# Optimization experiments

Hardware: AMD Instinct MI355X
Metric: run time of the kernel (lower is better)

Reference implementation:

```python
import jax, jax.numpy as jnp
import numpy as np

D_MODEL = 512
NUM_HEADS = 8
HEAD_DIM = D_MODEL // NUM_HEADS
LN_EPS = 1e-5


def setup_inputs() -> dict:
    key = jax.random.key(0)
    ks = jax.random.split(key, 12)
    B, S, D = 4, 8192, D_MODEL
    scale = 1.0 / np.sqrt(D)  # xavier-ish init
    inp = {
        "x": jax.random.normal(ks[0], (B, S, D), dtype=jnp.float32),
        "Wq": jax.random.normal(ks[1], (D, D), dtype=jnp.float32) * scale,
        "bq": jnp.zeros((D,), dtype=jnp.float32),
        "Wk": jax.random.normal(ks[2], (D, D), dtype=jnp.float32) * scale,
        "bk": jnp.zeros((D,), dtype=jnp.float32),
        "Wv": jax.random.normal(ks[3], (D, D), dtype=jnp.float32) * scale,
        "bv": jnp.zeros((D,), dtype=jnp.float32),
        "Wo": jax.random.normal(ks[4], (D, D), dtype=jnp.float32) * scale,
        "bo": jnp.zeros((D,), dtype=jnp.float32),
        "gamma": jnp.ones((D,), dtype=jnp.float32),
        "beta": jnp.zeros((D,), dtype=jnp.float32),
    }
    return inp


def _split_heads(t, B, S):
    # (B, S, D) -> (B, H, S, hd)
    return t.reshape(B, S, NUM_HEADS, HEAD_DIM).transpose(0, 2, 1, 3)


def _feature_map(t):
    return jax.nn.elu(t) + 1.0


def reference(x, Wq, bq, Wk, bk, Wv, bv, Wo, bo, gamma, beta):
    B, S, D = x.shape
    q = _split_heads(x @ Wq + bq, B, S)
    k = _split_heads(x @ Wk + bk, B, S)
    v = _split_heads(x @ Wv + bv, B, S)

    q = _feature_map(q)
    k = _feature_map(k)

    # kv summary: (B, H, hd, hd) -- O(n d^2) instead of O(n^2 d)
    kv = jnp.einsum('bhnd,bhnm->bhdm', k, v)
    out = jnp.einsum('bhnd,bhdm->bhnm', q, kv)

    k_sum = k.sum(axis=2)  # (B, H, hd)
    normalizer = jnp.clip(jnp.einsum('bhnd,bhd->bhn', q, k_sum), 1e-6, None)
    out = out / normalizer[..., None]

    # merge heads: (B, H, S, hd) -> (B, S, D)
    out = out.transpose(0, 2, 1, 3).reshape(B, S, D)
    out = out @ Wo + bo

    # residual + layer norm (dropout is identity in eval / p=0)
    y = x + out
    mean = y.mean(axis=-1, keepdims=True)
    var = y.var(axis=-1, keepdims=True)
    y = (y - mean) * jax.lax.rsqrt(var + LN_EPS)
    return y * gamma + beta
```

## Files before the change

kernel.cpp:

```cpp
#include <hip/hip_runtime.h>
#include <cstdint>

#define SEQ     8192
#define BATCH   4
#define NHEAD   8
#define NTOK    (BATCH*SEQ)

typedef __bf16 bf16x8 __attribute__((ext_vector_type(8)));
typedef float  floatx4 __attribute__((ext_vector_type(4)));

static __device__ __forceinline__ uint16_t f2b(float f) {
    uint32_t u = __float_as_uint(f);
    u += 0x7fffu + ((u >> 16) & 1u);
    return (uint16_t)(u >> 16);
}

static __device__ __forceinline__ void async_copy16(const uint16_t* g, uint16_t* l) {
#if __has_builtin(__builtin_amdgcn_global_load_lds)
    __builtin_amdgcn_global_load_lds(
        (const __attribute__((address_space(1))) void*)g,
        (__attribute__((address_space(3))) void*)l, 16, 0, 0);
#else
    *(uint4*)l = *(const uint4*)g;
#endif
}

__global__ __launch_bounds__(256) void convert_x(
    const float* __restrict__ X, uint16_t* __restrict__ Xb)
{
    const size_t i = ((size_t)blockIdx.x * 256 + threadIdx.x) * 8;
    float4 f0 = *(const float4*)(X + i);
    float4 f1 = *(const float4*)(X + i + 4);
    uint4 o;
    uint16_t* p = (uint16_t*)&o;
    p[0]=f2b(f0.x); p[1]=f2b(f0.y); p[2]=f2b(f0.z); p[3]=f2b(f0.w);
    p[4]=f2b(f1.x); p[5]=f2b(f1.y); p[6]=f2b(f1.z); p[7]=f2b(f1.w);
    *(uint4*)(Xb + i) = o;
}

__global__ __launch_bounds__(256) void convert_w(
    const float* __restrict__ Wq, const float* __restrict__ Wk,
    const float* __restrict__ Wv, const float* __restrict__ Wo,
    uint16_t* __restrict__ out)
{
    const int z = blockIdx.z;
    const float* W = (z == 0) ? Wq : (z == 1) ? Wk : (z == 2) ? Wv : Wo;
    uint16_t* o = out + (size_t)z * 262144;
    const int n0 = blockIdx.x * 64, k0 = blockIdx.y * 64;
    __shared__ uint16_t tl[64][64];
    const int t = threadIdx.x;
    const int r  = t >> 4;
    const int c4 = (t & 15) * 4;
    #pragma unroll
    for (int s = 0; s < 4; ++s) {
        const int k = r + s * 16;
        float4 f = *(const float4*)(W + (size_t)(k0 + k) * 512 + n0 + c4);
        tl[c4 + 0][k] = f2b(f.x); tl[c4 + 1][k] = f2b(f.y);
        tl[c4 + 2][k] = f2b(f.z); tl[c4 + 3][k] = f2b(f.w);
    }
    __syncthreads();
    const int n  = t >> 2;
    const int kk = (t & 3) * 16;
    uint4* dst = (uint4*)(o + (size_t)(n0 + n) * 512 + k0 + kk);
    dst[0] = *(const uint4*)&tl[n][kk];
    dst[1] = *(const uint4*)&tl[n][kk + 8];
}

__global__ __launch_bounds__(256) void qkv128(
    const uint16_t* __restrict__ Xb,
    const uint16_t* __restrict__ Wt,
    const float* __restrict__ bq_, const float* __restrict__ bk_,
    const float* __restrict__ bv_,
    uint16_t* __restrict__ outQ, uint16_t* __restrict__ outK,
    uint16_t* __restrict__ outV)
{
    const int id = blockIdx.x;
    const int c  = id & 7;
    const int r_ = id >> 3;
    const int j_ = r_ % 12;
    const int s  = (r_ / 12) * 8 + c;
    const int proj = j_ >> 2;
    const int n0   = (j_ & 3) * 128;
    const int m0   = s * 128;

    const uint16_t* W = Wt + (size_t)proj * 262144;
    const float* bias = (proj == 0) ? bq_ : (proj == 1) ? bk_ : bv_;
    uint16_t* out     = (proj == 0) ? outQ : (proj == 1) ? outK : outV;
    const int act = (proj < 2);

    __shared__ uint16_t sA[128 * 32];
    __shared__ uint16_t sB[128 * 32];
    const int t = threadIdx.x;
    const int wave = t >> 6, lane = t & 63, quad = lane >> 4, lrow = lane & 15;
    const int wm = (wave & 1) * 64, wn = (wave >> 1) * 64;
    const int sr = t >> 2;
    const int sc = (t & 3) * 8;

    floatx4 acc[4][4] = {};

    for (int k0 = 0; k0 < 512; k0 += 32) {
        const uint16_t* gA = Xb + (size_t)(m0 + sr) * 512 + k0 + sc;
        async_copy16(gA, sA + t * 8);
        async_copy16(gA + 64 * 512, sA + (t + 256) * 8);
        const uint16_t* gB = W + (size_t)(n0 + sr) * 512 + k0 + sc;
        async_copy16(gB, sB + t * 8);
        async_copy16(gB + 64 * 512, sB + (t + 256) * 8);
        __syncthreads();
        bf16x8 af[4], bfr[4];
        #pragma unroll
        for (int i = 0; i < 4; ++i)
            af[i] = *(const bf16x8*)(sA + (wm + i * 16 + lrow) * 32 + quad * 8);
        #pragma unroll
        for (int j = 0; j < 4; ++j)
            bfr[j] = *(const bf16x8*)(sB + (wn + j * 16 + lrow) * 32 + quad * 8);
        #pragma unroll
        for (int i = 0; i < 4; ++i)
            #pragma unroll
            for (int j = 0; j < 4; ++j)
                acc[i][j] = __builtin_amdgcn_mfma_f32_16x16x32_bf16(af[i], bfr[j], acc[i][j], 0, 0, 0);
        __syncthreads();
    }

    #pragma unroll
    for (int j = 0; j < 4; ++j) {
        const int col = n0 + wn + j * 16 + lrow;
        const float bb = bias[col];
        #pragma unroll
        for (int i = 0; i < 4; ++i) {
            #pragma unroll
            for (int r = 0; r < 4; ++r) {
                const int row = m0 + wm + i * 16 + quad * 4 + r;
                float v = acc[i][j][r] + bb;
                if (act) v = (v > 0.0f) ? (v + 1.0f) : __expf(v);
                out[(size_t)row * 512 + col] = f2b(v);
            }
        }
    }
}

__global__ __launch_bounds__(256) void kv_accum(
    const uint16_t* __restrict__ K,
    const uint16_t* __restrict__ V,
    float* __restrict__ KV,
    float* __restrict__ KSUM)
{
    const int chunk = blockIdx.x;
    const int h     = blockIdx.y;
    const int b     = blockIdx.z;
    const int t    = threadIdx.x;
    const int wv   = t >> 6;
    const int lane = t & 63;
    const int quad = lane >> 4;
    const int lrow = lane & 15;

    __shared__ uint16_t kt[64 * 72];
    __shared__ uint16_t vt[64 * 72];

    floatx4 acc[4] = {};
    floatx4 accS = {};
    union { uint16_t u[8]; bf16x8 v; } one_u;
    #pragma unroll
    for (int j = 0; j < 8; ++j) one_u.u[j] = 0x3F80;
    const bf16x8 ones = one_u.v;

    const size_t base = ((size_t)(b * SEQ + chunk * 512)) * 512 + h * 64;

    for (int n0 = 0; n0 < 512; n0 += 64) {
        #pragma unroll
        for (int s = 0; s < 2; ++s) {
            const int i   = t + 256 * s;
            const int tok = i >> 3;
            const int d0  = (i & 7) * 8;
            uint4 kq = *(const uint4*)(K + base + (size_t)(n0 + tok) * 512 + d0);
            const uint16_t* kp = (const uint16_t*)&kq;
            #pragma unroll
            for (int j = 0; j < 8; ++j) kt[(d0 + j) * 72 + tok] = kp[j];
            uint4 vq = *(const uint4*)(V + base + (size_t)(n0 + tok) * 512 + d0);
            const uint16_t* vp = (const uint16_t*)&vq;
            #pragma unroll
            for (int j = 0; j < 8; ++j) vt[(d0 + j) * 72 + tok] = vp[j];
        }
        __syncthreads();
        #pragma unroll
        for (int ks = 0; ks < 2; ++ks) {
            bf16x8 af = *(const bf16x8*)(kt + (wv * 16 + lrow) * 72 + ks * 32 + quad * 8);
            accS = __builtin_amdgcn_mfma_f32_16x16x32_bf16(af, ones, accS, 0, 0, 0);
            #pragma unroll
            for (int nt = 0; nt < 4; ++nt) {
                bf16x8 bf = *(const bf16x8*)(vt + (nt * 16 + lrow) * 72 + ks * 32 + quad * 8);
                acc[nt] = __builtin_amdgcn_mfma_f32_16x16x32_bf16(af, bf, acc[nt], 0, 0, 0);
            }
        }
        __syncthreads();
    }

    float* kvp = KV + (size_t)(b * NHEAD + h) * 4096;
    #pragma unroll
    for (int nt = 0; nt < 4; ++nt) {
        const int m = nt * 16 + lrow;
        #pragma unroll
        for (int r = 0; r < 4; ++r) {
            const int d = wv * 16 + quad * 4 + r;
            atomicAdd(kvp + d * 64 + m, acc[nt][r]);
        }
    }
    if (lrow == 0) {
        float* kp = KSUM + (size_t)(b * NHEAD + h) * 64;
        #pragma unroll
        for (int r = 0; r < 4; ++r)
            atomicAdd(kp + wv * 16 + quad * 4 + r, accS[r]);
    }
}

__global__ __launch_bounds__(256) void attn_apply(
    const uint16_t* __restrict__ Q,
    const float* __restrict__ KVg,
    const float* __restrict__ KSg,
    uint16_t* __restrict__ OUT)
{
    const int h    = blockIdx.y;
    const int tok0 = blockIdx.x * 64;
    const int b    = tok0 >> 13;
    const int t    = threadIdx.x;
    const int wv   = t >> 6;
    const int lane = t & 63;
    const int quad = lane >> 4;
    const int lrow = lane & 15;

    __shared__ uint16_t bt[64 * 72];
    __shared__ uint16_t ksb[64];

    const float* kvp = KVg + (size_t)(b * NHEAD + h) * 4096;
    #pragma unroll
    for (int s = 0; s < 16; ++s) {
        const int e = t + 256 * s;
        const int d = e >> 6, m = e & 63;
        bt[m * 72 + d] = f2b(kvp[e]);
    }
    if (t < 64) ksb[t] = f2b(KSg[(size_t)(b * NHEAD + h) * 64 + t]);
    __syncthreads();

    floatx4 acc[4] = {};
    floatx4 accN = {};
    const uint16_t* qrow = Q + (size_t)(tok0 + wv * 16 + lrow) * 512 + h * 64 + quad * 8;
    #pragma unroll
    for (int ks = 0; ks < 2; ++ks) {
        bf16x8 af = *(const bf16x8*)(qrow + ks * 32);
        bf16x8 bks = *(const bf16x8*)(ksb + ks * 32 + quad * 8);
        accN = __builtin_amdgcn_mfma_f32_16x16x32_bf16(af, bks, accN, 0, 0, 0);
        #pragma unroll
        for (int nt = 0; nt < 4; ++nt) {
            bf16x8 bf = *(const bf16x8*)(bt + (nt * 16 + lrow) * 72 + ks * 32 + quad * 8);
            acc[nt] = __builtin_amdgcn_mfma_f32_16x16x32_bf16(af, bf, acc[nt], 0, 0, 0);
        }
    }

    #pragma unroll
    for (int r = 0; r < 4; ++r) {
        const float inv = 1.0f / fmaxf(accN[r], 1e-6f);
        const int tok = tok0 + wv * 16 + quad * 4 + r;
        #pragma unroll
        for (int nt = 0; nt < 4; ++nt)
            OUT[(size_t)tok * 512 + h * 64 + nt * 16 + lrow] = f2b(acc[nt][r] * inv);
    }
}

__global__ __launch_bounds__(256) void gemm_out_ln(
    const uint16_t* __restrict__ A,
    const uint16_t* __restrict__ Wt,
    const float* __restrict__ bias,
    const float* __restrict__ resid,
    const float* __restrict__ gamma,
    const float* __restrict__ beta,
    float* __restrict__ OUT)
{
    const int m0 = blockIdx.x * 64;

    __shared__ uint16_t sA[64 * 32];
    __shared__ uint16_t sB[512 * 32];
    __shared__ float rs[4][64], rs2[4][64];

    const int t = threadIdx.x;
    const int wave = t >> 6, lane = t & 63, quad = lane >> 4, lrow = lane & 15;
    const int wn = wave * 128;
    const int sr = t >> 2;
    const int sc = (t & 3) * 8;

    floatx4 acc[4][8] = {};

    for (int k0 = 0; k0 < 512; k0 += 32) {
        const uint16_t* gA = A + (size_t)(m0 + sr) * 512 + k0 + sc;
        async_copy16(gA, sA + t * 8);
        const uint16_t* gB = Wt + (size_t)sr * 512 + k0 + sc;
        #pragma unroll
        for (int s = 0; s < 8; ++s)
            async_copy16(gB + s * 32768, sB + t * 8 + s * 2048);
        __syncthreads();
        bf16x8 af[4], bfr[8];
        #pragma unroll
        for (int i = 0; i < 4; ++i)
            af[i] = *(const bf16x8*)(sA + (i * 16 + lrow) * 32 + quad * 8);
        #pragma unroll
        for (int j = 0; j < 8; ++j)
            bfr[j] = *(const bf16x8*)(sB + (wn + j * 16 + lrow) * 32 + quad * 8);
        #pragma unroll
        for (int i = 0; i < 4; ++i)
            #pragma unroll
            for (int j = 0; j < 8; ++j)
                acc[i][j] = __builtin_amdgcn_mfma_f32_16x16x32_bf16(af[i], bfr[j], acc[i][j], 0, 0, 0);
        __syncthreads();
    }

    float g[8], be[8], bb[8];
    #pragma unroll
    for (int j = 0; j < 8; ++j) {
        const int col = wn + j * 16 + lrow;
        bb[j] = bias[col];
        g[j]  = gamma[col];
        be[j] = beta[col];
    }
    #pragma unroll
    for (int i = 0; i < 4; ++i) {
        #pragma unroll
        for (int r = 0; r < 4; ++r) {
            const int row = i * 16 + quad * 4 + r;
            const float* rp = resid + (size_t)(m0 + row) * 512 + wn;
            #pragma unroll
            for (int j = 0; j < 8; ++j)
                acc[i][j][r] += bb[j] + rp[j * 16 + lrow];
        }
    }

    #pragma unroll
    for (int i = 0; i < 4; ++i) {
        #pragma unroll
        for (int r = 0; r < 4; ++r) {
            const int row = i * 16 + quad * 4 + r;
            float s = 0.f, s2 = 0.f;
            #pragma unroll
            for (int j = 0; j < 8; ++j) {
                const float v = acc[i][j][r];
                s += v; s2 += v * v;
            }
            #pragma unroll
            for (int off = 8; off > 0; off >>= 1) {
                s  += __shfl_xor(s, off, 64);
                s2 += __shfl_xor(s2, off, 64);
            }
            if (lrow == 0) { rs[wave][row] = s; rs2[wave][row] = s2; }
        }
    }
    __syncthreads();

    #pragma unroll
    for (int i = 0; i < 4; ++i) {
        #pragma unroll
        for (int r = 0; r < 4; ++r) {
            const int row = i * 16 + quad * 4 + r;
            const float tot  = rs[0][row] + rs[1][row] + rs[2][row] + rs[3][row];
            const float tot2 = rs2[0][row] + rs2[1][row] + rs2[2][row] + rs2[3][row];
            const float mean = tot * (1.0f / 512.0f);
            const float var  = tot2 * (1.0f / 512.0f) - mean * mean;
            const float inv  = rsqrtf(var + 1e-5f);
            float* op = OUT + (size_t)(m0 + row) * 512 + wn;
            #pragma unroll
            for (int j = 0; j < 8; ++j)
                op[j * 16 + lrow] = (acc[i][j][r] - mean) * inv * g[j] + be[j];
        }
    }
}

extern "C" void kernel_launch(void* const* d_in, const int* in_sizes, int n_in,
                              void* d_out, int out_size, void* d_ws, size_t ws_size,
                              hipStream_t stream)
{
    (void)in_sizes; (void)n_in; (void)out_size; (void)ws_size;
    const float* x     = (const float*)d_in[0];
    const float* Wq    = (const float*)d_in[1];
    const float* bq    = (const float*)d_in[2];
    const float* Wk    = (const float*)d_in[3];
    const float* bk    = (const float*)d_in[4];
    const float* Wv    = (const float*)d_in[5];
    const float* bv    = (const float*)d_in[6];
    const float* Wo    = (const float*)d_in[7];
    const float* bo    = (const float*)d_in[8];
    const float* gamma = (const float*)d_in[9];
    const float* beta  = (const float*)d_in[10];

    uint8_t* ws = (uint8_t*)d_ws;
    float*    KV   = (float*)ws;
    float*    KSUM = (float*)(ws + (size_t)32 * 4096 * 4);
    uint16_t* Wt   = (uint16_t*)(ws + (size_t)32 * 4096 * 4 + 32 * 64 * 4);
    uint16_t* phiQ = (uint16_t*)(ws + (size_t)32 * 4096 * 4 + 32 * 64 * 4
                                    + (size_t)4 * 262144 * 2);
    uint16_t* Xb   = phiQ + (size_t)NTOK * 512;
    uint16_t* phiK = (uint16_t*)d_out;
    uint16_t* vbuf = (uint16_t*)d_out + (size_t)NTOK * 512;
    uint16_t* attn = Xb;

    hipMemsetAsync(ws, 0, (size_t)32 * 4096 * 4 + 32 * 64 * 4, stream);

    dim3 blk(256);
    convert_x<<<dim3(NTOK * 512 / (256 * 8)), blk, 0, stream>>>(x, Xb);
    convert_w<<<dim3(8, 8, 4), blk, 0, stream>>>(Wq, Wk, Wv, Wo, Wt);
    qkv128<<<dim3(3072), blk, 0, stream>>>(
        Xb, Wt, bq, bk, bv, phiQ, phiK, vbuf);
    kv_accum<<<dim3(16, NHEAD, BATCH), blk, 0, stream>>>(phiK, vbuf, KV, KSUM);
    attn_apply<<<dim3(NTOK / 64, NHEAD), blk, 0, stream>>>(phiQ, KV, KSUM, attn);
    gemm_out_ln<<<dim3(512), blk, 0, stream>>>(
        attn, Wt + (size_t)3 * 262144, bo, x, gamma, beta, (float*)d_out);
}
```

Baseline: 318.7 us.

## Stage GEMM and attention outputs through swizzled LDS for coalesced 16-byte stores

The QKV projection kernel now loads a 64-wide K slab per iteration (halving barrier count) into a unified shared buffer. It then writes its bf16 results into that buffer with an XOR swizzle and stores them to global memory as coalesced 16-byte vectors instead of scattered 2-byte stores. The attention-apply kernel does the same output staging through its existing LDS buffer. This cuts uncoalesced narrow global writes at the cost of extra LDS traffic, barriers and a larger LDS footprint that may lower occupancy.

```diff
diff --git a/kernel.cpp b/kernel.cpp
--- a/kernel.cpp
+++ b/kernel.cpp
@@ -88,8 +88,7 @@
     uint16_t* out     = (proj == 0) ? outQ : (proj == 1) ? outK : outV;
     const int act = (proj < 2);
 
-    __shared__ uint16_t sA[128 * 32];
-    __shared__ uint16_t sB[128 * 32];
+    __shared__ uint16_t smem[128 * 128];
     const int t = threadIdx.x;
     const int wave = t >> 6, lane = t & 63, quad = lane >> 4, lrow = lane & 15;
     const int wm = (wave & 1) * 64, wn = (wave >> 1) * 64;
@@ -98,43 +97,59 @@
 
     floatx4 acc[4][4] = {};
 
-    for (int k0 = 0; k0 < 512; k0 += 32) {
+    for (int k0 = 0; k0 < 512; k0 += 64) {
         const uint16_t* gA = Xb + (size_t)(m0 + sr) * 512 + k0 + sc;
-        async_copy16(gA, sA + t * 8);
-        async_copy16(gA + 64 * 512, sA + (t + 256) * 8);
+        async_copy16(gA,            smem + t * 8);
+        async_copy16(gA + 64 * 512, smem + (t + 256) * 8);
+        async_copy16(gA + 32,            smem + 4096 + t * 8);
+        async_copy16(gA + 64 * 512 + 32, smem + 4096 + (t + 256) * 8);
         const uint16_t* gB = W + (size_t)(n0 + sr) * 512 + k0 + sc;
-        async_copy16(gB, sB + t * 8);
-        async_copy16(gB + 64 * 512, sB + (t + 256) * 8);
-        __syncthreads();
-        bf16x8 af[4], bfr[4];
-        #pragma unroll
-        for (int i = 0; i < 4; ++i)
-            af[i] = *(const bf16x8*)(sA + (wm + i * 16 + lrow) * 32 + quad * 8);
-        #pragma unroll
-        for (int j = 0; j < 4; ++j)
-            bfr[j] = *(const bf16x8*)(sB + (wn + j * 16 + lrow) * 32 + quad * 8);
-        #pragma unroll
-        for (int i = 0; i < 4; ++i)
+        async_copy16(gB,            smem + 8192 + t * 8);
+        async_copy16(gB + 64 * 512, smem + 8192 + (t + 256) * 8);
+        async_copy16(gB + 32,            smem + 12288 + t * 8);
+        async_copy16(gB + 64 * 512 + 32, smem + 12288 + (t + 256) * 8);
+        __syncthreads();
+        #pragma unroll
+        for (int h = 0; h < 2; ++h) {
+            bf16x8 af[4], bfr[4];
+            #pragma unroll
+            for (int i = 0; i < 4; ++i)
+                af[i] = *(const bf16x8*)(smem + h * 4096 + (wm + i * 16 + lrow) * 32 + quad * 8);
             #pragma unroll
             for (int j = 0; j < 4; ++j)
-                acc[i][j] = __builtin_amdgcn_mfma_f32_16x16x32_bf16(af[i], bfr[j], acc[i][j], 0, 0, 0);
+                bfr[j] = *(const bf16x8*)(smem + 8192 + h * 4096 + (wn + j * 16 + lrow) * 32 + quad * 8);
+            #pragma unroll
+            for (int i = 0; i < 4; ++i)
+                #pragma unroll
+                for (int j = 0; j < 4; ++j)
+                    acc[i][j] = __builtin_amdgcn_mfma_f32_16x16x32_bf16(af[i], bfr[j], acc[i][j], 0, 0, 0);
+        }
         __syncthreads();
     }
 
     #pragma unroll
     for (int j = 0; j < 4; ++j) {
-        const int col = n0 + wn + j * 16 + lrow;
-        const float bb = bias[col];
+        const int col = wn + j * 16 + lrow;
+        const float bb = bias[n0 + col];
         #pragma unroll
         for (int i = 0; i < 4; ++i) {
             #pragma unroll
             for (int r = 0; r < 4; ++r) {
-                const int row = m0 + wm + i * 16 + quad * 4 + r;
+                const int row = wm + i * 16 + quad * 4 + r;
                 float v = acc[i][j][r] + bb;
                 if (act) v = (v > 0.0f) ? (v + 1.0f) : __expf(v);
-                out[(size_t)row * 512 + col] = f2b(v);
+                smem[row * 128 + (col ^ (((row >> 2) & 3) << 4))] = f2b(v);
             }
         }
+    }
+    __syncthreads();
+    #pragma unroll
+    for (int p = 0; p < 8; ++p) {
+        const int idx = p * 256 + t;
+        const int row = idx >> 4;
+        const int cc  = (idx & 15) * 8;
+        uint4 v = *(const uint4*)(smem + row * 128 + (cc ^ (((row >> 2) & 3) << 4)));
+        *(uint4*)(out + (size_t)(m0 + row) * 512 + n0 + cc) = v;
     }
 }
 
@@ -255,13 +270,25 @@
         }
     }
 
+    __syncthreads();
     #pragma unroll
     for (int r = 0; r < 4; ++r) {
         const float inv = 1.0f / fmaxf(accN[r], 1e-6f);
-        const int tok = tok0 + wv * 16 + quad * 4 + r;
-        #pragma unroll
-        for (int nt = 0; nt < 4; ++nt)
-            OUT[(size_t)tok * 512 + h * 64 + nt * 16 + lrow] = f2b(acc[nt][r] * inv);
+        const int row = wv * 16 + quad * 4 + r;
+        #pragma unroll
+        for (int nt = 0; nt < 4; ++nt) {
+            const int col = nt * 16 + lrow;
+            bt[row * 64 + (col ^ (((row >> 2) & 3) << 4))] = f2b(acc[nt][r] * inv);
+        }
+    }
+    __syncthreads();
+    #pragma unroll
+    for (int p = 0; p < 2; ++p) {
+        const int idx = p * 256 + t;
+        const int row = idx >> 3;
+        const int cc  = (idx & 7) * 8;
+        uint4 v = *(const uint4*)(bt + row * 64 + (cc ^ (((row >> 2) & 3) << 4)));
+        *(uint4*)(OUT + (size_t)(tok0 + row) * 512 + h * 64 + cc) = v;
     }
 }
 
```

Result: no change. 314.6 us (-1.3%).
